# Optimization experiments

Hardware: AMD Instinct MI355X
Metric: run time of the kernel (lower is better)

## Reference

```python
import jax, jax.numpy as jnp
import numpy as np

N_NODES = 40000
N_EDGES = 640000
IN_CH = 128
HID_CH = 128
BN_EPS = 1e-5


def setup_inputs() -> dict:
    key = jax.random.key(0)
    k_x, k_ei, k_w, k_g = jax.random.split(key, 4)
    x = jax.random.normal(k_x, (N_NODES, IN_CH), dtype=jnp.float32)
    edge_index = jax.random.randint(k_ei, (2, N_EDGES), 0, N_NODES, dtype=jnp.int32)
    # Glorot init for GCNConv weight, zero bias (PyG defaults)
    limit = float(np.sqrt(6.0 / (IN_CH + HID_CH)))
    W = jax.random.uniform(k_w, (IN_CH, HID_CH), dtype=jnp.float32, minval=-limit, maxval=limit)
    b = jnp.zeros((HID_CH,), dtype=jnp.float32)
    gamma = jnp.ones((HID_CH,), dtype=jnp.float32)
    beta = jnp.zeros((HID_CH,), dtype=jnp.float32)
    return {"x": x, "edge_index": edge_index, "W": W, "b": b, "gamma": gamma, "beta": beta}


def reference(x, edge_index, W, b, gamma, beta):
    N = x.shape[0]
    src, dst = edge_index[0], edge_index[1]

    # --- GCNConv: h = x @ W, symmetric-normalized aggregation with self-loops ---
    h = x @ W  # [N, H]
    ones = jnp.ones((src.shape[0],), dtype=x.dtype)
    deg = jax.ops.segment_sum(ones, dst, num_segments=N) + 1.0  # +1 for self-loop
    dinv = jax.lax.rsqrt(deg)  # deg >= 1 always
    norm = dinv[src] * dinv[dst]  # [E]
    msg = h[src] * norm[:, None]  # [E, H] gather
    agg = jax.ops.segment_sum(msg, dst, num_segments=N)  # scatter-add
    agg = agg + h * (dinv * dinv)[:, None]  # self-loop contribution
    out = agg + b  # bias added after aggregation (PyG GCNConv)

    # --- BatchNorm1d (training mode: batch stats, biased variance) ---
    mean = jnp.mean(out, axis=0)
    var = jnp.mean((out - mean) ** 2, axis=0)
    out = gamma * (out - mean) * jax.lax.rsqrt(var + BN_EPS) + beta

    # --- ReLU (dropout is a no-op in eval) ---
    return jax.nn.relu(out)
```

## Files before the change

kernel.cpp:

```cpp
#include <hip/hip_runtime.h>

#define N_NODES 40000
#define N_EDGES 640000
#define CH 128
#define BN_EPS 1e-5f
#define CAP 64
#define MM_ROWS 32
#define MM_BLOCKS (N_NODES / MM_ROWS)
#define FILL_BLOCKS (N_EDGES / 1024)


__device__ __forceinline__ float bf_lo(unsigned u) { return __uint_as_float(u << 16); }
__device__ __forceinline__ float bf_hi(unsigned u) { return __uint_as_float(u & 0xffff0000u); }
__device__ __forceinline__ unsigned short f2bf(float f) {
    unsigned u = __float_as_uint(f);
    unsigned r = 0x7fffu + ((u >> 16) & 1u);
    return (unsigned short)((u + r) >> 16);
}
__device__ __forceinline__ unsigned pack2bf(float a, float b) {
    return (unsigned)f2bf(a) | ((unsigned)f2bf(b) << 16);
}

__global__ __launch_bounds__(256) void mm_fill_kernel(const float* __restrict__ x,
                                                      const float* __restrict__ W,
                                                      unsigned short* __restrict__ hbf,
                                                      const int* __restrict__ src,
                                                      const int* __restrict__ dst,
                                                      int* __restrict__ cnt,
                                                      unsigned short* __restrict__ bucket16) {
    __shared__ unsigned Wsb[CH * CH / 2];
    __shared__ unsigned xsb[CH * 16];
    int t = threadIdx.x;
    int bb = blockIdx.x;
    if (bb % 3 == 2) {
        int fi = bb / 3;
        int base = cnt[N_NODES];
        int4 dd = ((const int4*)dst)[fi * 256 + t];
        int4 ss = ((const int4*)src)[fi * 256 + t];
        int d[4] = {dd.x, dd.y, dd.z, dd.w};
        int s[4] = {ss.x, ss.y, ss.z, ss.w};
#pragma unroll
        for (int k = 0; k < 4; ++k) {
            int slot = atomicAdd(&cnt[d[k]], 1) - base;
            if (slot < CAP) bucket16[d[k] * CAP + slot] = (unsigned short)s[k];
        }
        return;
    }
    int mmIdx = (bb / 3) * 2 + (bb % 3);
    for (int i = t; i < CH * CH / 4; i += 256) {
        float4 w = ((const float4*)W)[i];
        uint2 p;
        p.x = pack2bf(w.x, w.y);
        p.y = pack2bf(w.z, w.w);
        ((uint2*)Wsb)[i] = p;
    }
    size_t row0 = (size_t)mmIdx * MM_ROWS;
    {
        int p = t >> 4;
        int k4a = t & 15;
#pragma unroll
        for (int kk = 0; kk < 2; ++kk) {
            int k4 = k4a + kk * 16;
            float4 xa = ((const float4*)(x + (row0 + p) * CH))[k4];
            float4 xb = ((const float4*)(x + (row0 + p + 16) * CH))[k4];
            xsb[(k4 * 4 + 0) * 16 + p] = pack2bf(xa.x, xb.x);
            xsb[(k4 * 4 + 1) * 16 + p] = pack2bf(xa.y, xb.y);
            xsb[(k4 * 4 + 2) * 16 + p] = pack2bf(xa.z, xb.z);
            xsb[(k4 * 4 + 3) * 16 + p] = pack2bf(xa.w, xb.w);
        }
    }
    __syncthreads();
    int ch4 = t & 31;
    int rg = t >> 5;
    float4 accA = {0,0,0,0}, accB = {0,0,0,0}, accC = {0,0,0,0}, accD = {0,0,0,0};
#pragma unroll 8
    for (int k = 0; k < CH; ++k) {
        uint2 wp = ((const uint2*)Wsb)[k * 32 + ch4];
        unsigned xpa = xsb[k * 16 + rg];
        unsigned xpb = xsb[k * 16 + rg + 8];
        float w0 = bf_lo(wp.x), w1 = bf_hi(wp.x), w2 = bf_lo(wp.y), w3 = bf_hi(wp.y);
        float xa0 = bf_lo(xpa), xa1 = bf_hi(xpa);
        float xb0 = bf_lo(xpb), xb1 = bf_hi(xpb);
        accA.x += xa0 * w0; accA.y += xa0 * w1; accA.z += xa0 * w2; accA.w += xa0 * w3;
        accB.x += xa1 * w0; accB.y += xa1 * w1; accB.z += xa1 * w2; accB.w += xa1 * w3;
        accC.x += xb0 * w0; accC.y += xb0 * w1; accC.z += xb0 * w2; accC.w += xb0 * w3;
        accD.x += xb1 * w0; accD.y += xb1 * w1; accD.z += xb1 * w2; accD.w += xb1 * w3;
    }
    uint2 o;
    o.x = pack2bf(accA.x, accA.y); o.y = pack2bf(accA.z, accA.w);
    ((uint2*)(hbf + (row0 + rg) * CH))[ch4] = o;
    o.x = pack2bf(accB.x, accB.y); o.y = pack2bf(accB.z, accB.w);
    ((uint2*)(hbf + (row0 + rg + 16) * CH))[ch4] = o;
    o.x = pack2bf(accC.x, accC.y); o.y = pack2bf(accC.z, accC.w);
    ((uint2*)(hbf + (row0 + rg + 8) * CH))[ch4] = o;
    o.x = pack2bf(accD.x, accD.y); o.y = pack2bf(accD.z, accD.w);
    ((uint2*)(hbf + (row0 + rg + 24) * CH))[ch4] = o;
}

__global__ __launch_bounds__(256) void aggregate_kernel(const unsigned short* __restrict__ bucket16,
                                                        const int* __restrict__ cnt,
                                                        const unsigned short* __restrict__ hbf,
                                                        const float* __restrict__ b,
                                                        float* __restrict__ out,
                                                        float* __restrict__ sums32) {
    __shared__ float bsum[CH], bsq[CH];
    int t = threadIdx.x;
    if (t < CH) { bsum[t] = 0.0f; bsq[t] = 0.0f; }
    __syncthreads();
    int base = cnt[N_NODES];
    int wid = t >> 6;
    int lane = t & 63;
    int quarter = lane >> 4;
    int ql = lane & 15;
    const uint4* h4 = (const uint4*)hbf;
    float4 bv0 = ((const float4*)b)[ql * 2];
    float4 bv1 = ((const float4*)b)[ql * 2 + 1];
    int n_base = blockIdx.x * 16 + wid * 4;
    float s0 = 0, s1 = 0, s2 = 0, s3 = 0, s4 = 0, s5 = 0, s6 = 0, s7 = 0;
    float q0 = 0, q1 = 0, q2 = 0, q3 = 0, q4 = 0, q5 = 0, q6 = 0, q7 = 0;
#pragma unroll 1
    for (int it = 0; it < 4; ++it) {
        int n = n_base + it;
        int cn = cnt[n] - base;
        int m = cn < CAP ? cn : CAP;
        float dn = rsqrtf((float)cn + 1.0f);
        unsigned sx_pre = (lane < m) ? (unsigned)bucket16[n * CAP + lane] : 0u;
        float a0 = 0, a1 = 0, a2 = 0, a3 = 0, a4 = 0, a5 = 0, a6 = 0, a7 = 0;
        for (int jj = 0; jj < m; jj += 16) {
            int e = jj + quarter * 4;
            unsigned sx0 = (unsigned)__shfl((int)sx_pre, e, 64);
            unsigned sx1 = (unsigned)__shfl((int)sx_pre, e + 1, 64);
            unsigned sx2 = (unsigned)__shfl((int)sx_pre, e + 2, 64);
            unsigned sx3 = (unsigned)__shfl((int)sx_pre, e + 3, 64);
            int c0g = cnt[sx0];
            int c1g = cnt[sx1];
            int c2g = cnt[sx2];
            int c3g = cnt[sx3];
            uint4 r0 = h4[(size_t)sx0 * 16 + ql];
            uint4 r1 = h4[(size_t)sx1 * 16 + ql];
            uint4 r2 = h4[(size_t)sx2 * 16 + ql];
            uint4 r3 = h4[(size_t)sx3 * 16 + ql];
            float d0 = (e     < m) ? rsqrtf((float)(c0g - base) + 1.0f) : 0.0f;
            float d1 = (e + 1 < m) ? rsqrtf((float)(c1g - base) + 1.0f) : 0.0f;
            float d2 = (e + 2 < m) ? rsqrtf((float)(c2g - base) + 1.0f) : 0.0f;
            float d3 = (e + 3 < m) ? rsqrtf((float)(c3g - base) + 1.0f) : 0.0f;
            a0 += bf_lo(r0.x) * d0; a1 += bf_hi(r0.x) * d0;
            a2 += bf_lo(r0.y) * d0; a3 += bf_hi(r0.y) * d0;
            a4 += bf_lo(r0.z) * d0; a5 += bf_hi(r0.z) * d0;
            a6 += bf_lo(r0.w) * d0; a7 += bf_hi(r0.w) * d0;
            a0 += bf_lo(r1.x) * d1; a1 += bf_hi(r1.x) * d1;
            a2 += bf_lo(r1.y) * d1; a3 += bf_hi(r1.y) * d1;
            a4 += bf_lo(r1.z) * d1; a5 += bf_hi(r1.z) * d1;
            a6 += bf_lo(r1.w) * d1; a7 += bf_hi(r1.w) * d1;
            a0 += bf_lo(r2.x) * d2; a1 += bf_hi(r2.x) * d2;
            a2 += bf_lo(r2.y) * d2; a3 += bf_hi(r2.y) * d2;
            a4 += bf_lo(r2.z) * d2; a5 += bf_hi(r2.z) * d2;
            a6 += bf_lo(r2.w) * d2; a7 += bf_hi(r2.w) * d2;
            a0 += bf_lo(r3.x) * d3; a1 += bf_hi(r3.x) * d3;
            a2 += bf_lo(r3.y) * d3; a3 += bf_hi(r3.y) * d3;
            a4 += bf_lo(r3.z) * d3; a5 += bf_hi(r3.z) * d3;
            a6 += bf_lo(r3.w) * d3; a7 += bf_hi(r3.w) * d3;
        }
        a0 += __shfl_xor(a0, 16, 64); a0 += __shfl_xor(a0, 32, 64);
        a1 += __shfl_xor(a1, 16, 64); a1 += __shfl_xor(a1, 32, 64);
        a2 += __shfl_xor(a2, 16, 64); a2 += __shfl_xor(a2, 32, 64);
        a3 += __shfl_xor(a3, 16, 64); a3 += __shfl_xor(a3, 32, 64);
        a4 += __shfl_xor(a4, 16, 64); a4 += __shfl_xor(a4, 32, 64);
        a5 += __shfl_xor(a5, 16, 64); a5 += __shfl_xor(a5, 32, 64);
        a6 += __shfl_xor(a6, 16, 64); a6 += __shfl_xor(a6, 32, 64);
        a7 += __shfl_xor(a7, 16, 64); a7 += __shfl_xor(a7, 32, 64);
        if (quarter == 0) {
            uint4 raw = h4[(size_t)n * 16 + ql];
            float sq = dn * dn;
            float o0 = a0 * dn + bf_lo(raw.x) * sq + bv0.x;
            float o1 = a1 * dn + bf_hi(raw.x) * sq + bv0.y;
            float o2 = a2 * dn + bf_lo(raw.y) * sq + bv0.z;
            float o3 = a3 * dn + bf_hi(raw.y) * sq + bv0.w;
            float o4 = a4 * dn + bf_lo(raw.z) * sq + bv1.x;
            float o5 = a5 * dn + bf_hi(raw.z) * sq + bv1.y;
            float o6 = a6 * dn + bf_lo(raw.w) * sq + bv1.z;
            float o7 = a7 * dn + bf_hi(raw.w) * sq + bv1.w;
            float4* op = (float4*)(out + (size_t)n * CH + ql * 8);
            float4 w0 = {o0, o1, o2, o3};
            float4 w1 = {o4, o5, o6, o7};
            op[0] = w0;
            op[1] = w1;
            s0 += o0; q0 += o0 * o0;
            s1 += o1; q1 += o1 * o1;
            s2 += o2; q2 += o2 * o2;
            s3 += o3; q3 += o3 * o3;
            s4 += o4; q4 += o4 * o4;
            s5 += o5; q5 += o5 * o5;
            s6 += o6; q6 += o6 * o6;
            s7 += o7; q7 += o7 * o7;
        }
    }
    if (quarter == 0) {
        int c0 = ql * 8;
        atomicAdd(&bsum[c0 + 0], s0); atomicAdd(&bsq[c0 + 0], q0);
        atomicAdd(&bsum[c0 + 1], s1); atomicAdd(&bsq[c0 + 1], q1);
        atomicAdd(&bsum[c0 + 2], s2); atomicAdd(&bsq[c0 + 2], q2);
        atomicAdd(&bsum[c0 + 3], s3); atomicAdd(&bsq[c0 + 3], q3);
        atomicAdd(&bsum[c0 + 4], s4); atomicAdd(&bsq[c0 + 4], q4);
        atomicAdd(&bsum[c0 + 5], s5); atomicAdd(&bsq[c0 + 5], q5);
        atomicAdd(&bsum[c0 + 6], s6); atomicAdd(&bsq[c0 + 6], q6);
        atomicAdd(&bsum[c0 + 7], s7); atomicAdd(&bsq[c0 + 7], q7);
    }
    __syncthreads();
    atomicAdd(&sums32[(blockIdx.x & 31) * 256 + t], (t < CH) ? bsum[t] : bsq[t - CH]);
}

__global__ __launch_bounds__(256) void bn_relu_kernel(float* __restrict__ out,
                                                      const float* __restrict__ sums32,
                                                      const float* __restrict__ gamma,
                                                      const float* __restrict__ beta) {
    __shared__ float sc[CH], sh[CH];
    int t = threadIdx.x;
    if (t < CH) {
        float P = sums32[32 * 256];
        float s = -32.0f * P, q = -32.0f * P;
#pragma unroll
        for (int k = 0; k < 32; ++k) {
            s += sums32[k * 256 + t];
            q += sums32[k * 256 + CH + t];
        }
        const float invN = 1.0f / (float)N_NODES;
        float mean = s * invN;
        float var = q * invN - mean * mean;
        float scale = gamma[t] * rsqrtf(var + BN_EPS);
        sc[t] = scale;
        sh[t] = beta[t] - mean * scale;
    }
    __syncthreads();
    int i = blockIdx.x * 256 + t;
    int c0 = (i & 31) * 4;
    float4 v = ((float4*)out)[i];
    float r0 = v.x * sc[c0] + sh[c0];
    float r1 = v.y * sc[c0 + 1] + sh[c0 + 1];
    float r2 = v.z * sc[c0 + 2] + sh[c0 + 2];
    float r3 = v.w * sc[c0 + 3] + sh[c0 + 3];
    v.x = r0 > 0.0f ? r0 : 0.0f;
    v.y = r1 > 0.0f ? r1 : 0.0f;
    v.z = r2 > 0.0f ? r2 : 0.0f;
    v.w = r3 > 0.0f ? r3 : 0.0f;
    ((float4*)out)[i] = v;
}

extern "C" void kernel_launch(void* const* d_in, const int* in_sizes, int n_in,
                              void* d_out, int out_size, void* d_ws, size_t ws_size,
                              hipStream_t stream) {
    const float* x = (const float*)d_in[0];
    const int* ei = (const int*)d_in[1];
    const float* W = (const float*)d_in[2];
    const float* b = (const float*)d_in[3];
    const float* gamma = (const float*)d_in[4];
    const float* beta = (const float*)d_in[5];
    float* out = (float*)d_out;
    const int* src = ei;
    const int* dst = ei + N_EDGES;
    char* ws = (char*)d_ws;

    unsigned short* hbf = (unsigned short*)ws;
    int* cnt = (int*)(ws + 10240000);
    float* sums32 = (float*)(ws + 10400256);
    unsigned short* bucket16 = (unsigned short*)(ws + 10433280);

    mm_fill_kernel<<<MM_BLOCKS + FILL_BLOCKS, 256, 0, stream>>>(x, W, hbf, src, dst, cnt,
                                                                bucket16);
    aggregate_kernel<<<N_NODES / 16, 256, 0, stream>>>(bucket16, cnt, hbf, b, out, sums32);
    bn_relu_kernel<<<N_NODES * CH / 4 / 256, 256, 0, stream>>>(out, sums32, gamma, beta);
}
```

Baseline: 167.0 us.

## Use bf16 MFMA for the x@W projection with larger row tiles

Replaces the scalar FMA matmul in the fused projection/bucket-fill kernel with the 16x16x32 bf16 MFMA instruction. W fragments are held in registers and x rows are streamed directly from global memory. Rows per block grow from 32 to 160, so the W conversion and staging cost is spread over more rows. Matmul blocks are no longer interleaved with fill blocks but placed first in the grid. Risks are fewer matmul blocks, which lowers parallelism, and scattered 2-byte stores of h.

Result: no change. 165.1 us (-1.1%).

```diff
diff --git a/kernel.cpp b/kernel.cpp
--- a/kernel.cpp
+++ b/kernel.cpp
@@ -5,10 +5,13 @@
 #define CH 128
 #define BN_EPS 1e-5f
 #define CAP 64
-#define MM_ROWS 32
+#define MM_ROWS 160
 #define MM_BLOCKS (N_NODES / MM_ROWS)
 #define FILL_BLOCKS (N_EDGES / 1024)
 
+
+typedef __bf16 bf16x8 __attribute__((ext_vector_type(8)));
+typedef float f32x4 __attribute__((ext_vector_type(4)));
 
 __device__ __forceinline__ float bf_lo(unsigned u) { return __uint_as_float(u << 16); }
 __device__ __forceinline__ float bf_hi(unsigned u) { return __uint_as_float(u & 0xffff0000u); }
@@ -28,12 +31,11 @@
                                                       const int* __restrict__ dst,
                                                       int* __restrict__ cnt,
                                                       unsigned short* __restrict__ bucket16) {
-    __shared__ unsigned Wsb[CH * CH / 2];
-    __shared__ unsigned xsb[CH * 16];
+    __shared__ uint4 Wsb4[2048];
     int t = threadIdx.x;
     int bb = blockIdx.x;
-    if (bb % 3 == 2) {
-        int fi = bb / 3;
+    if (bb >= MM_BLOCKS) {
+        int fi = bb - MM_BLOCKS;
         int base = cnt[N_NODES];
         int4 dd = ((const int4*)dst)[fi * 256 + t];
         int4 ss = ((const int4*)src)[fi * 256 + t];
@@ -46,55 +48,58 @@
         }
         return;
     }
-    int mmIdx = (bb / 3) * 2 + (bb % 3);
-    for (int i = t; i < CH * CH / 4; i += 256) {
-        float4 w = ((const float4*)W)[i];
-        uint2 p;
-        p.x = pack2bf(w.x, w.y);
-        p.y = pack2bf(w.z, w.w);
-        ((uint2*)Wsb)[i] = p;
-    }
-    size_t row0 = (size_t)mmIdx * MM_ROWS;
-    {
-        int p = t >> 4;
-        int k4a = t & 15;
-#pragma unroll
-        for (int kk = 0; kk < 2; ++kk) {
-            int k4 = k4a + kk * 16;
-            float4 xa = ((const float4*)(x + (row0 + p) * CH))[k4];
-            float4 xb = ((const float4*)(x + (row0 + p + 16) * CH))[k4];
-            xsb[(k4 * 4 + 0) * 16 + p] = pack2bf(xa.x, xb.x);
-            xsb[(k4 * 4 + 1) * 16 + p] = pack2bf(xa.y, xb.y);
-            xsb[(k4 * 4 + 2) * 16 + p] = pack2bf(xa.z, xb.z);
-            xsb[(k4 * 4 + 3) * 16 + p] = pack2bf(xa.w, xb.w);
-        }
-    }
-    __syncthreads();
-    int ch4 = t & 31;
-    int rg = t >> 5;
-    float4 accA = {0,0,0,0}, accB = {0,0,0,0}, accC = {0,0,0,0}, accD = {0,0,0,0};
-#pragma unroll 8
-    for (int k = 0; k < CH; ++k) {
-        uint2 wp = ((const uint2*)Wsb)[k * 32 + ch4];
-        unsigned xpa = xsb[k * 16 + rg];
-        unsigned xpb = xsb[k * 16 + rg + 8];
-        float w0 = bf_lo(wp.x), w1 = bf_hi(wp.x), w2 = bf_lo(wp.y), w3 = bf_hi(wp.y);
-        float xa0 = bf_lo(xpa), xa1 = bf_hi(xpa);
-        float xb0 = bf_lo(xpb), xb1 = bf_hi(xpb);
-        accA.x += xa0 * w0; accA.y += xa0 * w1; accA.z += xa0 * w2; accA.w += xa0 * w3;
-        accB.x += xa1 * w0; accB.y += xa1 * w1; accB.z += xa1 * w2; accB.w += xa1 * w3;
-        accC.x += xb0 * w0; accC.y += xb0 * w1; accC.z += xb0 * w2; accC.w += xb0 * w3;
-        accD.x += xb1 * w0; accD.y += xb1 * w1; accD.z += xb1 * w2; accD.w += xb1 * w3;
-    }
-    uint2 o;
-    o.x = pack2bf(accA.x, accA.y); o.y = pack2bf(accA.z, accA.w);
-    ((uint2*)(hbf + (row0 + rg) * CH))[ch4] = o;
-    o.x = pack2bf(accB.x, accB.y); o.y = pack2bf(accB.z, accB.w);
-    ((uint2*)(hbf + (row0 + rg + 16) * CH))[ch4] = o;
-    o.x = pack2bf(accC.x, accC.y); o.y = pack2bf(accC.z, accC.w);
-    ((uint2*)(hbf + (row0 + rg + 8) * CH))[ch4] = o;
-    o.x = pack2bf(accD.x, accD.y); o.y = pack2bf(accD.z, accD.w);
-    ((uint2*)(hbf + (row0 + rg + 24) * CH))[ch4] = o;
+#pragma unroll
+    for (int it = 0; it < 8; ++it) {
+        int task = it * 256 + t;
+        int n = task & 127;
+        int k8 = task >> 7;
+        const float* wp = W + (size_t)(k8 * 8) * CH + n;
+        float w0 = wp[0 * CH], w1 = wp[1 * CH], w2 = wp[2 * CH], w3 = wp[3 * CH];
+        float w4 = wp[4 * CH], w5 = wp[5 * CH], w6 = wp[6 * CH], w7 = wp[7 * CH];
+        uint4 u;
+        u.x = pack2bf(w0, w1); u.y = pack2bf(w2, w3);
+        u.z = pack2bf(w4, w5); u.w = pack2bf(w6, w7);
+        int ks = k8 >> 2, q = k8 & 3, ct = n >> 4;
+        Wsb4[(ct * 4 + ks) * 64 + q * 16 + (n & 15)] = u;
+    }
+    __syncthreads();
+    int w = t >> 6, l = t & 63;
+    int q = l >> 4, c15 = l & 15;
+    int ct0 = 2 * w, ct1 = 2 * w + 1;
+    bf16x8 bf0[4], bf1[4];
+#pragma unroll
+    for (int ks = 0; ks < 4; ++ks) {
+        bf0[ks] = __builtin_bit_cast(bf16x8, Wsb4[(ct0 * 4 + ks) * 64 + l]);
+        bf1[ks] = __builtin_bit_cast(bf16x8, Wsb4[(ct1 * 4 + ks) * 64 + l]);
+    }
+    size_t row0 = (size_t)bb * MM_ROWS;
+    for (int rt = 0; rt < MM_ROWS / 16; ++rt) {
+        const float4* xr = (const float4*)(x + (row0 + rt * 16 + c15) * CH);
+        float4 xf[8];
+#pragma unroll
+        for (int ks = 0; ks < 4; ++ks) {
+            xf[2 * ks]     = xr[ks * 8 + 2 * q];
+            xf[2 * ks + 1] = xr[ks * 8 + 2 * q + 1];
+        }
+        f32x4 acc0 = {0.f, 0.f, 0.f, 0.f};
+        f32x4 acc1 = {0.f, 0.f, 0.f, 0.f};
+#pragma unroll
+        for (int ks = 0; ks < 4; ++ks) {
+            float4 f0 = xf[2 * ks], f1 = xf[2 * ks + 1];
+            uint4 ua;
+            ua.x = pack2bf(f0.x, f0.y); ua.y = pack2bf(f0.z, f0.w);
+            ua.z = pack2bf(f1.x, f1.y); ua.w = pack2bf(f1.z, f1.w);
+            bf16x8 af = __builtin_bit_cast(bf16x8, ua);
+            acc0 = __builtin_amdgcn_mfma_f32_16x16x32_bf16(af, bf0[ks], acc0, 0, 0, 0);
+            acc1 = __builtin_amdgcn_mfma_f32_16x16x32_bf16(af, bf1[ks], acc1, 0, 0, 0);
+        }
+        unsigned short* hr = hbf + (row0 + rt * 16 + q * 4) * CH;
+#pragma unroll
+        for (int r = 0; r < 4; ++r) {
+            hr[r * CH + ct0 * 16 + c15] = f2bf(acc0[r]);
+            hr[r * CH + ct1 * 16 + c15] = f2bf(acc1[r]);
+        }
+    }
 }
 
 __global__ __launch_bounds__(256) void aggregate_kernel(const unsigned short* __restrict__ bucket16,
```
